# Kernel optimization log

Hardware: AMD Instinct MI355X
Metric: run time of the kernel (lower is better)

Reference implementation:

```python
import jax, jax.numpy as jnp
import numpy as np

E = 640000
N_AGENTS = 50000
D = 128
NUM_S = 50000


def setup_inputs() -> dict:
    key = jax.random.key(0)
    k1, k2, k3 = jax.random.split(key, 3)
    edge_weights = jax.random.uniform(k1, (E,), dtype=jnp.float32)
    agent_features = jax.random.normal(k2, (N_AGENTS, D), dtype=jnp.float32)
    edge_index = jax.random.randint(k3, (2, E), 0, NUM_S, dtype=jnp.int64)
    return {
        "edge_weights": edge_weights,
        "agent_features": agent_features,
        "edge_index": edge_index,
        "num_s": NUM_S,
    }


def reference(edge_weights, agent_features, edge_index, num_s):
    s_idx = edge_index[0]
    a_idx = edge_index[1]
    # gather per-edge agent features: [E, D]
    eaf = agent_features[a_idx]
    # weighted scatter-add: per-source feature sums [num_s, D] and weight sums [num_s]
    sum_wf = jax.ops.segment_sum(edge_weights[:, None] * eaf, s_idx, num_segments=num_s)
    sum_w = jax.ops.segment_sum(edge_weights, s_idx, num_segments=num_s)
    mean_per_s = sum_wf / (sum_w[:, None] + 1e-8)
    # second pass: weighted squared deviation per edge, scattered per source
    sq_diff = jnp.sum((eaf - mean_per_s[s_idx]) ** 2, axis=1)  # [E]
    var_per_s = jax.ops.segment_sum(edge_weights * sq_diff, s_idx, num_segments=num_s)
    valid = sum_w > 0
    n_valid = jnp.sum(valid)
    loss = jnp.sum(jnp.where(valid, var_per_s, 0.0)) / jnp.maximum(n_valid, 1).astype(var_per_s.dtype)
    return jnp.where(n_valid > 0, loss, jnp.asarray(0.0, var_per_s.dtype))
```

## Files before the change

### kernel.cpp

```cpp
#include <hip/hip_runtime.h>
#include <hip/hip_fp16.h>


#define D  128
#define NS 50000
#define KMAX 64
#define NBINS 391
#define BIN_CAP 2048

typedef unsigned long long ull;
typedef float f32x2 __attribute__((ext_vector_type(2)));


__global__ void prep_kernel(const float* __restrict__ af, unsigned char* __restrict__ af_q,
                            float* __restrict__ sqnorm, float* __restrict__ accum,
                            int* __restrict__ done, unsigned* __restrict__ binCursor,
                            int num_a) {
    int gtid   = blockIdx.x * 256 + threadIdx.x;
    int stride = gridDim.x * 256;
    if (gtid == 0) { accum[0] = 0.f; accum[1] = 0.f; *done = 0; }
    for (int b = gtid; b < NBINS; b += stride)
        binCursor[b * 16] = (unsigned)b * BIN_CAP;

    for (int u = gtid; u < num_a * 16; u += stride) {
        int a    = u >> 4;
        int comp = (u & 15) << 3;
        const float* src = af + (size_t)a * D + comp;
        float4 v0 = *reinterpret_cast<const float4*>(src);
        float4 v1 = *reinterpret_cast<const float4*>(src + 4);
        unsigned lo = __builtin_amdgcn_cvt_pk_fp8_f32(v0.x, v0.y, 0u, false);
        lo = __builtin_amdgcn_cvt_pk_fp8_f32(v0.z, v0.w, lo, true);
        unsigned hi = __builtin_amdgcn_cvt_pk_fp8_f32(v1.x, v1.y, 0u, false);
        hi = __builtin_amdgcn_cvt_pk_fp8_f32(v1.z, v1.w, hi, true);
        int p  = comp >> 6;
        int cc = comp & 63;
        *reinterpret_cast<ull*>(af_q + ((size_t)p * num_a + a) * 64 + cc) =
            ((ull)hi << 32) | (ull)lo;

        f32x2 q0 = __builtin_amdgcn_cvt_pk_f32_fp8(lo, false);
        f32x2 q1 = __builtin_amdgcn_cvt_pk_f32_fp8(lo, true);
        f32x2 q2 = __builtin_amdgcn_cvt_pk_f32_fp8(hi, false);
        f32x2 q3 = __builtin_amdgcn_cvt_pk_f32_fp8(hi, true);
        float ss = q0.x*q0.x + q0.y*q0.y + q1.x*q1.x + q1.y*q1.y
                 + q2.x*q2.x + q2.y*q2.y + q3.x*q3.x + q3.y*q3.y;
        #pragma unroll
        for (int m = 1; m <= 8; m <<= 1) ss += __shfl_xor(ss, m, 64);
        if ((u & 15) == 0) sqnorm[a] = ss;
    }
}


__global__ __launch_bounds__(256) void bin_pass(
    const int* __restrict__ s_idx,
    const int* __restrict__ a_idx,
    const float* __restrict__ ew,
    unsigned* __restrict__ binCursor,
    ull* __restrict__ coarse, int E)
{
    __shared__ unsigned hist[NBINS];
    __shared__ unsigned base[NBINS];
    int nb    = gridDim.x;
    int chunk = (E + nb - 1) / nb;
    int e0    = blockIdx.x * chunk;
    int e1    = min(E, e0 + chunk);

    for (int t = threadIdx.x; t < NBINS; t += 256) hist[t] = 0;
    __syncthreads();
    for (int i = e0 + (int)threadIdx.x; i < e1; i += 256)
        atomicAdd(&hist[(unsigned)s_idx[i] >> 7], 1u);
    __syncthreads();
    for (int t = threadIdx.x; t < NBINS; t += 256) {
        unsigned c = hist[t];
        base[t] = c ? atomicAdd(&binCursor[t * 16], c) : 0u;
        hist[t] = 0;
    }
    __syncthreads();
    for (int i = e0 + (int)threadIdx.x; i < e1; i += 256) {
        int s = s_idx[i];
        unsigned bin = (unsigned)s >> 7;
        unsigned r   = atomicAdd(&hist[bin], 1u);
        unsigned pos = base[bin] + r;
        if (pos < (bin + 1) * BIN_CAP) {
            unsigned low = ((unsigned)a_idx[i] << 16)
                         | (unsigned)__half_as_ushort(__float2half(ew[i]));
            coarse[pos] = ((ull)((unsigned)s & 127u) << 32) | (ull)low;
        }
    }
}


__global__ __launch_bounds__(256) void final_bucket(
    const ull* __restrict__ coarse,
    const unsigned* __restrict__ binCursor,
    unsigned* __restrict__ bucket, int* __restrict__ cnt, int num_s)
{
    __shared__ unsigned lcnt[128];
    int b = blockIdx.x;
    if (threadIdx.x < 128) lcnt[threadIdx.x] = 0;
    __syncthreads();
    unsigned start = (unsigned)b * BIN_CAP;
    unsigned end   = min(binCursor[b * 16], start + BIN_CAP);
    for (unsigned i = start + threadIdx.x; i < end; i += 256) {
        ull e = coarse[i];
        unsigned s7 = (unsigned)(e >> 32);
        unsigned r  = atomicAdd(&lcnt[s7], 1u);
        if (r < KMAX) {
            int s = b * 128 + (int)s7;
            bucket[((size_t)s << 6) + r] = (unsigned)e;
        }
    }
    __syncthreads();
    if (threadIdx.x < 128) {
        int s = b * 128 + (int)threadIdx.x;
        if (s < num_s) cnt[s] = (int)lcnt[threadIdx.x];
    }
}

__device__ __forceinline__ void fma16(const uint4& x, float w, float* acc) {
    f32x2 t;
    t = __builtin_amdgcn_cvt_pk_f32_fp8(x.x, false); acc[0]  += w*t.x; acc[1]  += w*t.y;
    t = __builtin_amdgcn_cvt_pk_f32_fp8(x.x, true);  acc[2]  += w*t.x; acc[3]  += w*t.y;
    t = __builtin_amdgcn_cvt_pk_f32_fp8(x.y, false); acc[4]  += w*t.x; acc[5]  += w*t.y;
    t = __builtin_amdgcn_cvt_pk_f32_fp8(x.y, true);  acc[6]  += w*t.x; acc[7]  += w*t.y;
    t = __builtin_amdgcn_cvt_pk_f32_fp8(x.z, false); acc[8]  += w*t.x; acc[9]  += w*t.y;
    t = __builtin_amdgcn_cvt_pk_f32_fp8(x.z, true);  acc[10] += w*t.x; acc[11] += w*t.y;
    t = __builtin_amdgcn_cvt_pk_f32_fp8(x.w, false); acc[12] += w*t.x; acc[13] += w*t.y;
    t = __builtin_amdgcn_cvt_pk_f32_fp8(x.w, true);  acc[14] += w*t.x; acc[15] += w*t.y;
}


__global__ __launch_bounds__(256) void slice_merged(
    const unsigned char* __restrict__ af_q,
    const float* __restrict__ sqnorm,
    const unsigned* __restrict__ bucket,
    const int* __restrict__ cnt,
    float* __restrict__ fn2a, float* __restrict__ fn2b,
    float* __restrict__ s2acc, float* __restrict__ wsumv,
    int num_s, int num_a)
{
    const bool p0  = (blockIdx.x & 1u) == 0u;
    const unsigned char* afp = af_q + (p0 ? 0 : (size_t)num_a * 64);
    int lblk    = blockIdx.x >> 1;
    int gid     = lblk * 256 + threadIdx.x;
    int group   = gid >> 5;
    int lane    = threadIdx.x & 31;
    int j       = lane >> 2;
    int ccq     = lane & 3;
    int ngroups = ((gridDim.x >> 1) * 256) >> 5;

    for (int s0 = group * 2; s0 < num_s; s0 += ngroups * 2) {
        int s1 = s0 + 1;
        int2 c2 = *reinterpret_cast<const int2*>(cnt + s0);
        int c0 = min(c2.x, KMAX);
        int c1 = min(c2.y, KMAX);
        const unsigned* b0 = bucket + ((size_t)s0 << 6);
        const unsigned* b1 = bucket + ((size_t)s1 << 6);

        float accA[16] = {};
        float accB[16] = {};
        float s2A = 0.f, wlA = 0.f, s2B = 0.f, wlB = 0.f;

        int cmax  = max(c0, c1);
        int iters = (cmax + 15) >> 4;
        for (int it = 0; it < iters; ++it) {
            int idxA = it * 16 + j;
            int idxB = idxA + 8;
            unsigned wa0  = (idxA < c0) ? b0[idxA] : 0u;
            unsigned wa0b = (idxB < c0) ? b0[idxB] : 0u;
            unsigned wa1  = (idxA < c1) ? b1[idxA] : 0u;
            unsigned wa1b = (idxB < c1) ? b1[idxB] : 0u;
            float w0  = __half2float(__ushort_as_half((unsigned short)(wa0  & 0xFFFFu)));
            float w0b = __half2float(__ushort_as_half((unsigned short)(wa0b & 0xFFFFu)));
            float w1  = __half2float(__ushort_as_half((unsigned short)(wa1  & 0xFFFFu)));
            float w1b = __half2float(__ushort_as_half((unsigned short)(wa1b & 0xFFFFu)));
            int A0  = (int)(wa0  >> 16);
            int A0b = (int)(wa0b >> 16);
            int A1  = (int)(wa1  >> 16);
            int A1b = (int)(wa1b >> 16);
            uint4 x  = *reinterpret_cast<const uint4*>(afp + ((size_t)A0  << 6) + (ccq << 4));
            uint4 xb = *reinterpret_cast<const uint4*>(afp + ((size_t)A0b << 6) + (ccq << 4));
            uint4 y  = *reinterpret_cast<const uint4*>(afp + ((size_t)A1  << 6) + (ccq << 4));
            uint4 yb = *reinterpret_cast<const uint4*>(afp + ((size_t)A1b << 6) + (ccq << 4));
            fma16(x,  w0,  accA);
            fma16(xb, w0b, accA);
            fma16(y,  w1,  accB);
            fma16(yb, w1b, accB);
            if (p0 && ccq == 0) {
                s2A += w0 * sqnorm[A0] + w0b * sqnorm[A0b];  wlA += w0 + w0b;
                s2B += w1 * sqnorm[A1] + w1b * sqnorm[A1b];  wlB += w1 + w1b;
            }
        }
        #pragma unroll
        for (int m = 4; m <= 16; m <<= 1) {
            #pragma unroll
            for (int k = 0; k < 16; ++k) {
                accA[k] += __shfl_xor(accA[k], m, 64);
                accB[k] += __shfl_xor(accB[k], m, 64);
            }
            if (p0) {
                s2A += __shfl_xor(s2A, m, 64); wlA += __shfl_xor(wlA, m, 64);
                s2B += __shfl_xor(s2B, m, 64); wlB += __shfl_xor(wlB, m, 64);
            }
        }
        float n2a = 0.f, n2b = 0.f;
        #pragma unroll
        for (int k = 0; k < 16; ++k) { n2a += accA[k] * accA[k]; n2b += accB[k] * accB[k]; }
        n2a += __shfl_xor(n2a, 1, 64); n2a += __shfl_xor(n2a, 2, 64);
        n2b += __shfl_xor(n2b, 1, 64); n2b += __shfl_xor(n2b, 2, 64);
        if (lane == 0) {
            if (p0) {
                fn2a[s0] = n2a;  s2acc[s0] = s2A;  wsumv[s0] = wlA;
                fn2a[s1] = n2b;  s2acc[s1] = s2B;  wsumv[s1] = wlB;
            } else {
                fn2b[s0] = n2a;
                fn2b[s1] = n2b;
            }
        }
    }
}


__global__ void loss_finalize(const float* __restrict__ fn2a, const float* __restrict__ fn2b,
                              const float* __restrict__ s2acc, const float* __restrict__ wsumv,
                              float* __restrict__ accum, int* __restrict__ done,
                              float* __restrict__ out, int num_s) {
    __shared__ float sv[4], sc[4];
    float lv = 0.f, lc = 0.f;
    for (int s = blockIdx.x * blockDim.x + threadIdx.x; s < num_s; s += gridDim.x * blockDim.x) {
        float w = wsumv[s];
        if (w > 0.f) {
            float n2  = fn2a[s] + fn2b[s];
            float inv = 1.f / (w + 1e-8f);
            lv += s2acc[s] - n2 * inv * (2.f - w * inv);
            lc += 1.f;
        }
    }
    #pragma unroll
    for (int m = 1; m < 64; m <<= 1) { lv += __shfl_xor(lv, m, 64); lc += __shfl_xor(lc, m, 64); }
    int wv = threadIdx.x >> 6;
    if ((threadIdx.x & 63) == 0) { sv[wv] = lv; sc[wv] = lc; }
    __syncthreads();
    if (threadIdx.x == 0) {
        atomicAdd(accum + 0, sv[0] + sv[1] + sv[2] + sv[3]);
        atomicAdd(accum + 1, sc[0] + sc[1] + sc[2] + sc[3]);
        __threadfence();
        unsigned t = atomicAdd((unsigned*)done, 1u);
        if (t == gridDim.x - 1) {
            float v = atomicAdd(accum + 0, 0.f);
            float c = atomicAdd(accum + 1, 0.f);
            out[0] = (c > 0.f) ? (v / fmaxf(c, 1.f)) : 0.f;
        }
    }
}

extern "C" void kernel_launch(void* const* d_in, const int* in_sizes, int n_in,
                              void* d_out, int out_size, void* d_ws, size_t ws_size,
                              hipStream_t stream) {
    const float* ew = (const float*)d_in[0];
    const float* af = (const float*)d_in[1];
    const int*   ei = (const int*)d_in[2];
    const int E     = in_sizes[0];
    const int num_a = in_sizes[1] / D;
    const int num_s = NS;

    const int* s_idx = ei;
    const int* a_idx = ei + E;

    char* ws = (char*)d_ws;
    size_t off = 0;
    auto alloc = [&](size_t bytes, size_t align) -> char* {
        off = (off + align - 1) & ~(align - 1);
        char* p = ws + off;
        off += bytes;
        return p;
    };
    int*   cnt    = (int*)alloc((size_t)(num_s + 4) * 4, 16);
    float* accum  = (float*)(cnt + num_s);
    int*   done   = (int*)(cnt + num_s + 2);
    float* fn2a   = (float*)alloc((size_t)num_s * 4, 16);
    float* fn2b   = (float*)alloc((size_t)num_s * 4, 16);
    float* s2acc  = (float*)alloc((size_t)num_s * 4, 16);
    float* wsumv  = (float*)alloc((size_t)num_s * 4, 16);
    float* sqnorm = (float*)alloc((size_t)num_a * 4, 16);
    unsigned* binCursor = (unsigned*)alloc((size_t)NBINS * 16 * 4, 64);
    unsigned char* af_q = (unsigned char*)alloc((size_t)2 * num_a * 64, 256);
    unsigned* bucket = (unsigned*)alloc((size_t)num_s * KMAX * 4, 512);
    ull* coarse = (ull*)alloc((size_t)NBINS * BIN_CAP * 8, 512);

    prep_kernel<<<(num_a * 16 + 255) / 256, 256, 0, stream>>>(af, af_q, sqnorm, accum, done,
                                                              binCursor, num_a);
    bin_pass<<<256, 256, 0, stream>>>(s_idx, a_idx, ew, binCursor, coarse, E);
    final_bucket<<<NBINS, 256, 0, stream>>>(coarse, binCursor, bucket, cnt, num_s);
    slice_merged<<<4096, 256, 0, stream>>>(af_q, sqnorm, bucket, cnt,
                                           fn2a, fn2b, s2acc, wsumv, num_s, num_a);
    loss_finalize<<<128, 256, 0, stream>>>(fn2a, fn2b, s2acc, wsumv, accum, done,
                                           (float*)d_out, num_s);
}
```

Baseline: 79.51 us.

## Fuse final bucketing into slice kernel via shared-memory counting sort per bin

Removes the separate final_bucket kernel and the global bucket/cnt arrays. Each bin_slice block reloads its coarse bin, counting-sorts entries by source in LDS with a wave prefix scan, and then accumulates features straight from shared memory. This drops a launch and a global write/read round trip, and also lifts the per-source KMAX cap. In exchange, both half-blocks of a bin redo the sort, and the grid shrinks from 4096 to 782 blocks, which may reduce latency hiding for the gathers.

```diff
diff --git a/kernel.cpp b/kernel.cpp
--- a/kernel.cpp
+++ b/kernel.cpp
@@ -4,7 +4,6 @@
 
 #define D  128
 #define NS 50000
-#define KMAX 64
 #define NBINS 391
 #define BIN_CAP 2048
 
@@ -88,34 +87,6 @@
     }
 }
 
-
-__global__ __launch_bounds__(256) void final_bucket(
-    const ull* __restrict__ coarse,
-    const unsigned* __restrict__ binCursor,
-    unsigned* __restrict__ bucket, int* __restrict__ cnt, int num_s)
-{
-    __shared__ unsigned lcnt[128];
-    int b = blockIdx.x;
-    if (threadIdx.x < 128) lcnt[threadIdx.x] = 0;
-    __syncthreads();
-    unsigned start = (unsigned)b * BIN_CAP;
-    unsigned end   = min(binCursor[b * 16], start + BIN_CAP);
-    for (unsigned i = start + threadIdx.x; i < end; i += 256) {
-        ull e = coarse[i];
-        unsigned s7 = (unsigned)(e >> 32);
-        unsigned r  = atomicAdd(&lcnt[s7], 1u);
-        if (r < KMAX) {
-            int s = b * 128 + (int)s7;
-            bucket[((size_t)s << 6) + r] = (unsigned)e;
-        }
-    }
-    __syncthreads();
-    if (threadIdx.x < 128) {
-        int s = b * 128 + (int)threadIdx.x;
-        if (s < num_s) cnt[s] = (int)lcnt[threadIdx.x];
-    }
-}
-
 __device__ __forceinline__ void fma16(const uint4& x, float w, float* acc) {
     f32x2 t;
     t = __builtin_amdgcn_cvt_pk_f32_fp8(x.x, false); acc[0]  += w*t.x; acc[1]  += w*t.y;
@@ -129,32 +100,65 @@
 }
 
 
-__global__ __launch_bounds__(256) void slice_merged(
+__global__ __launch_bounds__(256) void bin_slice(
+    const ull* __restrict__ coarse,
+    const unsigned* __restrict__ binCursor,
     const unsigned char* __restrict__ af_q,
     const float* __restrict__ sqnorm,
-    const unsigned* __restrict__ bucket,
-    const int* __restrict__ cnt,
     float* __restrict__ fn2a, float* __restrict__ fn2b,
     float* __restrict__ s2acc, float* __restrict__ wsumv,
     int num_s, int num_a)
 {
+    __shared__ unsigned sorted[BIN_CAP];
+    __shared__ unsigned lcnt[128];
+    __shared__ unsigned loff[128];
+    __shared__ unsigned lcur[128];
+
     const bool p0  = (blockIdx.x & 1u) == 0u;
+    const int  bin = blockIdx.x >> 1;
     const unsigned char* afp = af_q + (p0 ? 0 : (size_t)num_a * 64);
-    int lblk    = blockIdx.x >> 1;
-    int gid     = lblk * 256 + threadIdx.x;
-    int group   = gid >> 5;
-    int lane    = threadIdx.x & 31;
-    int j       = lane >> 2;
-    int ccq     = lane & 3;
-    int ngroups = ((gridDim.x >> 1) * 256) >> 5;
-
-    for (int s0 = group * 2; s0 < num_s; s0 += ngroups * 2) {
-        int s1 = s0 + 1;
-        int2 c2 = *reinterpret_cast<const int2*>(cnt + s0);
-        int c0 = min(c2.x, KMAX);
-        int c1 = min(c2.y, KMAX);
-        const unsigned* b0 = bucket + ((size_t)s0 << 6);
-        const unsigned* b1 = bucket + ((size_t)s1 << 6);
+    const int tid = threadIdx.x;
+
+    const unsigned start = (unsigned)bin * BIN_CAP;
+    const unsigned n = min(binCursor[bin * 16] - start, (unsigned)BIN_CAP);
+
+    if (tid < 128) lcnt[tid] = 0;
+    __syncthreads();
+    for (unsigned i = tid; i < n; i += 256)
+        atomicAdd(&lcnt[(unsigned)(coarse[start + i] >> 32)], 1u);
+    __syncthreads();
+    if (tid < 64) {
+        unsigned v0 = lcnt[tid], v1 = lcnt[64 + tid];
+        unsigned i0 = v0, i1 = v1;
+        #pragma unroll
+        for (int d = 1; d < 64; d <<= 1) {
+            unsigned t0 = __shfl_up(i0, d, 64);
+            unsigned t1 = __shfl_up(i1, d, 64);
+            if (tid >= d) { i0 += t0; i1 += t1; }
+        }
+        unsigned tot0 = __shfl(i0, 63, 64);
+        loff[tid]      = i0 - v0;         lcur[tid]      = i0 - v0;
+        loff[64 + tid] = tot0 + i1 - v1;  lcur[64 + tid] = tot0 + i1 - v1;
+    }
+    __syncthreads();
+    for (unsigned i = tid; i < n; i += 256) {
+        ull e = coarse[start + i];
+        unsigned r = atomicAdd(&lcur[(unsigned)(e >> 32)], 1u);
+        sorted[r] = (unsigned)e;
+    }
+    __syncthreads();
+
+    int group = tid >> 5;
+    int lane  = tid & 31;
+    int j     = lane >> 2;
+    int ccq   = lane & 3;
+
+    for (int p = 0; p < 8; ++p) {
+        int s7a = group * 16 + p * 2;
+        int sA  = bin * 128 + s7a;
+        if (sA >= num_s) break;
+        int c0 = (int)lcnt[s7a], c1 = (int)lcnt[s7a + 1];
+        int base0 = (int)loff[s7a], base1 = (int)loff[s7a + 1];
 
         float accA[16] = {};
         float accB[16] = {};
@@ -165,10 +169,10 @@
         for (int it = 0; it < iters; ++it) {
             int idxA = it * 16 + j;
             int idxB = idxA + 8;
-            unsigned wa0  = (idxA < c0) ? b0[idxA] : 0u;
-            unsigned wa0b = (idxB < c0) ? b0[idxB] : 0u;
-            unsigned wa1  = (idxA < c1) ? b1[idxA] : 0u;
-            unsigned wa1b = (idxB < c1) ? b1[idxB] : 0u;
+            unsigned wa0  = (idxA < c0) ? sorted[base0 + idxA] : 0u;
+            unsigned wa0b = (idxB < c0) ? sorted[base0 + idxB] : 0u;
+            unsigned wa1  = (idxA < c1) ? sorted[base1 + idxA] : 0u;
+            unsigned wa1b = (idxB < c1) ? sorted[base1 + idxB] : 0u;
             float w0  = __half2float(__ushort_as_half((unsigned short)(wa0  & 0xFFFFu)));
             float w0b = __half2float(__ushort_as_half((unsigned short)(wa0b & 0xFFFFu)));
             float w1  = __half2float(__ushort_as_half((unsigned short)(wa1  & 0xFFFFu)));
@@ -209,11 +213,11 @@
         n2b += __shfl_xor(n2b, 1, 64); n2b += __shfl_xor(n2b, 2, 64);
         if (lane == 0) {
             if (p0) {
-                fn2a[s0] = n2a;  s2acc[s0] = s2A;  wsumv[s0] = wlA;
-                fn2a[s1] = n2b;  s2acc[s1] = s2B;  wsumv[s1] = wlB;
+                fn2a[sA]     = n2a;  s2acc[sA]     = s2A;  wsumv[sA]     = wlA;
+                fn2a[sA + 1] = n2b;  s2acc[sA + 1] = s2B;  wsumv[sA + 1] = wlB;
             } else {
-                fn2b[s0] = n2a;
-                fn2b[s1] = n2b;
+                fn2b[sA]     = n2a;
+                fn2b[sA + 1] = n2b;
             }
         }
     }
@@ -274,9 +278,8 @@
         off += bytes;
         return p;
     };
-    int*   cnt    = (int*)alloc((size_t)(num_s + 4) * 4, 16);
-    float* accum  = (float*)(cnt + num_s);
-    int*   done   = (int*)(cnt + num_s + 2);
+    float* accum  = (float*)alloc(4 * 4, 16);
+    int*   done   = (int*)(accum + 2);
     float* fn2a   = (float*)alloc((size_t)num_s * 4, 16);
     float* fn2b   = (float*)alloc((size_t)num_s * 4, 16);
     float* s2acc  = (float*)alloc((size_t)num_s * 4, 16);
@@ -284,15 +287,13 @@
     float* sqnorm = (float*)alloc((size_t)num_a * 4, 16);
     unsigned* binCursor = (unsigned*)alloc((size_t)NBINS * 16 * 4, 64);
     unsigned char* af_q = (unsigned char*)alloc((size_t)2 * num_a * 64, 256);
-    unsigned* bucket = (unsigned*)alloc((size_t)num_s * KMAX * 4, 512);
     ull* coarse = (ull*)alloc((size_t)NBINS * BIN_CAP * 8, 512);
 
     prep_kernel<<<(num_a * 16 + 255) / 256, 256, 0, stream>>>(af, af_q, sqnorm, accum, done,
                                                               binCursor, num_a);
     bin_pass<<<256, 256, 0, stream>>>(s_idx, a_idx, ew, binCursor, coarse, E);
-    final_bucket<<<NBINS, 256, 0, stream>>>(coarse, binCursor, bucket, cnt, num_s);
-    slice_merged<<<4096, 256, 0, stream>>>(af_q, sqnorm, bucket, cnt,
-                                           fn2a, fn2b, s2acc, wsumv, num_s, num_a);
+    bin_slice<<<NBINS * 2, 256, 0, stream>>>(coarse, binCursor, af_q, sqnorm,
+                                             fn2a, fn2b, s2acc, wsumv, num_s, num_a);
     loss_finalize<<<128, 256, 0, stream>>>(fn2a, fn2b, s2acc, wsumv, accum, done,
                                            (float*)d_out, num_s);
 }
```

Result: slower. 88.47 us (+11.3%).

## Fuse prep and binning kernels, replace global bin cursors with per-block slots

Applied to the files above, without the earlier changes.

Merges the fp8 quantization prep kernel and the coarse binning pass into one launch: the first 256 blocks bin edges while the remaining blocks quantize agent features. Global atomic bin cursors are replaced by fixed per-(bin, block) slots of capacity 32 with a count table, which removes the cursor init and the global atomics. final_bucket now has each thread walk one block's slot serially. This saves a launch and the contention on shared cursors, but uses a larger coarse buffer, loses edges silently past 32 per slot, and gives final_bucket uneven per-thread serial loops.

```diff
diff --git a/kernel.cpp b/kernel.cpp
--- a/kernel.cpp
+++ b/kernel.cpp
@@ -6,84 +6,81 @@
 #define NS 50000
 #define KMAX 64
 #define NBINS 391
-#define BIN_CAP 2048
+#define CAP_PB 32
 
 typedef unsigned long long ull;
 typedef float f32x2 __attribute__((ext_vector_type(2)));
 
 
-__global__ void prep_kernel(const float* __restrict__ af, unsigned char* __restrict__ af_q,
-                            float* __restrict__ sqnorm, float* __restrict__ accum,
-                            int* __restrict__ done, unsigned* __restrict__ binCursor,
-                            int num_a) {
-    int gtid   = blockIdx.x * 256 + threadIdx.x;
-    int stride = gridDim.x * 256;
-    if (gtid == 0) { accum[0] = 0.f; accum[1] = 0.f; *done = 0; }
-    for (int b = gtid; b < NBINS; b += stride)
-        binCursor[b * 16] = (unsigned)b * BIN_CAP;
-
-    for (int u = gtid; u < num_a * 16; u += stride) {
-        int a    = u >> 4;
-        int comp = (u & 15) << 3;
-        const float* src = af + (size_t)a * D + comp;
-        float4 v0 = *reinterpret_cast<const float4*>(src);
-        float4 v1 = *reinterpret_cast<const float4*>(src + 4);
-        unsigned lo = __builtin_amdgcn_cvt_pk_fp8_f32(v0.x, v0.y, 0u, false);
-        lo = __builtin_amdgcn_cvt_pk_fp8_f32(v0.z, v0.w, lo, true);
-        unsigned hi = __builtin_amdgcn_cvt_pk_fp8_f32(v1.x, v1.y, 0u, false);
-        hi = __builtin_amdgcn_cvt_pk_fp8_f32(v1.z, v1.w, hi, true);
-        int p  = comp >> 6;
-        int cc = comp & 63;
-        *reinterpret_cast<ull*>(af_q + ((size_t)p * num_a + a) * 64 + cc) =
-            ((ull)hi << 32) | (ull)lo;
-
-        f32x2 q0 = __builtin_amdgcn_cvt_pk_f32_fp8(lo, false);
-        f32x2 q1 = __builtin_amdgcn_cvt_pk_f32_fp8(lo, true);
-        f32x2 q2 = __builtin_amdgcn_cvt_pk_f32_fp8(hi, false);
-        f32x2 q3 = __builtin_amdgcn_cvt_pk_f32_fp8(hi, true);
-        float ss = q0.x*q0.x + q0.y*q0.y + q1.x*q1.x + q1.y*q1.y
-                 + q2.x*q2.x + q2.y*q2.y + q3.x*q3.x + q3.y*q3.y;
-        #pragma unroll
-        for (int m = 1; m <= 8; m <<= 1) ss += __shfl_xor(ss, m, 64);
-        if ((u & 15) == 0) sqnorm[a] = ss;
-    }
-}
-
-
-__global__ __launch_bounds__(256) void bin_pass(
-    const int* __restrict__ s_idx,
-    const int* __restrict__ a_idx,
+__global__ __launch_bounds__(256) void prep_bin(
+    const float* __restrict__ af, unsigned char* __restrict__ af_q,
+    float* __restrict__ sqnorm, float* __restrict__ accum, int* __restrict__ done,
+    const int* __restrict__ s_idx, const int* __restrict__ a_idx,
     const float* __restrict__ ew,
-    unsigned* __restrict__ binCursor,
-    ull* __restrict__ coarse, int E)
+    unsigned* __restrict__ blkCnt,
+    ull* __restrict__ coarse,
+    int E, int num_a)
 {
     __shared__ unsigned hist[NBINS];
-    __shared__ unsigned base[NBINS];
-    int nb    = gridDim.x;
-    int chunk = (E + nb - 1) / nb;
-    int e0    = blockIdx.x * chunk;
-    int e1    = min(E, e0 + chunk);
-
-    for (int t = threadIdx.x; t < NBINS; t += 256) hist[t] = 0;
-    __syncthreads();
-    for (int i = e0 + (int)threadIdx.x; i < e1; i += 256)
-        atomicAdd(&hist[(unsigned)s_idx[i] >> 7], 1u);
-    __syncthreads();
-    for (int t = threadIdx.x; t < NBINS; t += 256) {
-        unsigned c = hist[t];
-        base[t] = c ? atomicAdd(&binCursor[t * 16], c) : 0u;
-        hist[t] = 0;
-    }
-    __syncthreads();
-    for (int i = e0 + (int)threadIdx.x; i < e1; i += 256) {
-        int s = s_idx[i];
-        unsigned bin = (unsigned)s >> 7;
-        unsigned r   = atomicAdd(&hist[bin], 1u);
-        unsigned pos = base[bin] + r;
-        if (pos < (bin + 1) * BIN_CAP) {
-            unsigned low = ((unsigned)a_idx[i] << 16)
-                         | (unsigned)__half_as_ushort(__float2half(ew[i]));
-            coarse[pos] = ((ull)((unsigned)s & 127u) << 32) | (ull)low;
+    const int tid = threadIdx.x;
+
+    if (blockIdx.x < 256) {
+        const int b     = blockIdx.x;
+        const int chunk = (E + 255) / 256;
+        const int e0    = b * chunk;
+        const int e1    = min(E, e0 + chunk);
+
+        for (int t = tid; t < NBINS; t += 256) hist[t] = 0;
+        __syncthreads();
+        for (int i = e0 + tid; i < e1; i += 256)
+            atomicAdd(&hist[(unsigned)s_idx[i] >> 7], 1u);
+        __syncthreads();
+        for (int t = tid; t < NBINS; t += 256) {
+            blkCnt[t * 256 + b] = min(hist[t], (unsigned)CAP_PB);
+            hist[t] = 0;
+        }
+        __syncthreads();
+        for (int i = e0 + tid; i < e1; i += 256) {
+            int s = s_idx[i];
+            unsigned bin = (unsigned)s >> 7;
+            unsigned r   = atomicAdd(&hist[bin], 1u);
+            if (r < CAP_PB) {
+                unsigned low = ((unsigned)a_idx[i] << 16)
+                             | (unsigned)__half_as_ushort(__float2half(ew[i]));
+                coarse[((size_t)bin * 256 + b) * CAP_PB + r] =
+                    ((ull)((unsigned)s & 127u) << 32) | (ull)low;
+            }
+        }
+    } else {
+        int pb     = blockIdx.x - 256;
+        int gtid   = pb * 256 + tid;
+        int stride = ((int)gridDim.x - 256) * 256;
+        if (gtid == 0) { accum[0] = 0.f; accum[1] = 0.f; *done = 0; }
+
+        for (int u = gtid; u < num_a * 16; u += stride) {
+            int a    = u >> 4;
+            int comp = (u & 15) << 3;
+            const float* src = af + (size_t)a * D + comp;
+            float4 v0 = *reinterpret_cast<const float4*>(src);
+            float4 v1 = *reinterpret_cast<const float4*>(src + 4);
+            unsigned lo = __builtin_amdgcn_cvt_pk_fp8_f32(v0.x, v0.y, 0u, false);
+            lo = __builtin_amdgcn_cvt_pk_fp8_f32(v0.z, v0.w, lo, true);
+            unsigned hi = __builtin_amdgcn_cvt_pk_fp8_f32(v1.x, v1.y, 0u, false);
+            hi = __builtin_amdgcn_cvt_pk_fp8_f32(v1.z, v1.w, hi, true);
+            int p  = comp >> 6;
+            int cc = comp & 63;
+            *reinterpret_cast<ull*>(af_q + ((size_t)p * num_a + a) * 64 + cc) =
+                ((ull)hi << 32) | (ull)lo;
+
+            f32x2 q0 = __builtin_amdgcn_cvt_pk_f32_fp8(lo, false);
+            f32x2 q1 = __builtin_amdgcn_cvt_pk_f32_fp8(lo, true);
+            f32x2 q2 = __builtin_amdgcn_cvt_pk_f32_fp8(hi, false);
+            f32x2 q3 = __builtin_amdgcn_cvt_pk_f32_fp8(hi, true);
+            float ss = q0.x*q0.x + q0.y*q0.y + q1.x*q1.x + q1.y*q1.y
+                     + q2.x*q2.x + q2.y*q2.y + q3.x*q3.x + q3.y*q3.y;
+            #pragma unroll
+            for (int m = 1; m <= 8; m <<= 1) ss += __shfl_xor(ss, m, 64);
+            if ((u & 15) == 0) sqnorm[a] = ss;
         }
     }
 }
@@ -91,28 +88,29 @@
 
 __global__ __launch_bounds__(256) void final_bucket(
     const ull* __restrict__ coarse,
-    const unsigned* __restrict__ binCursor,
+    const unsigned* __restrict__ blkCnt,
     unsigned* __restrict__ bucket, int* __restrict__ cnt, int num_s)
 {
     __shared__ unsigned lcnt[128];
-    int b = blockIdx.x;
-    if (threadIdx.x < 128) lcnt[threadIdx.x] = 0;
+    int bin = blockIdx.x;
+    int tid = threadIdx.x;
+    if (tid < 128) lcnt[tid] = 0;
     __syncthreads();
-    unsigned start = (unsigned)b * BIN_CAP;
-    unsigned end   = min(binCursor[b * 16], start + BIN_CAP);
-    for (unsigned i = start + threadIdx.x; i < end; i += 256) {
-        ull e = coarse[i];
+    unsigned c = blkCnt[bin * 256 + tid];
+    const ull* reg = coarse + ((size_t)bin * 256 + tid) * CAP_PB;
+    for (unsigned r = 0; r < c; ++r) {
+        ull e = reg[r];
         unsigned s7 = (unsigned)(e >> 32);
-        unsigned r  = atomicAdd(&lcnt[s7], 1u);
-        if (r < KMAX) {
-            int s = b * 128 + (int)s7;
-            bucket[((size_t)s << 6) + r] = (unsigned)e;
+        unsigned k  = atomicAdd(&lcnt[s7], 1u);
+        if (k < KMAX) {
+            int s = bin * 128 + (int)s7;
+            bucket[((size_t)s << 6) + k] = (unsigned)e;
         }
     }
     __syncthreads();
-    if (threadIdx.x < 128) {
-        int s = b * 128 + (int)threadIdx.x;
-        if (s < num_s) cnt[s] = (int)lcnt[threadIdx.x];
+    if (tid < 128) {
+        int s = bin * 128 + tid;
+        if (s < num_s) cnt[s] = (int)min(lcnt[tid], (unsigned)KMAX);
     }
 }
 
@@ -274,23 +272,24 @@
         off += bytes;
         return p;
     };
-    int*   cnt    = (int*)alloc((size_t)(num_s + 4) * 4, 16);
-    float* accum  = (float*)(cnt + num_s);
-    int*   done   = (int*)(cnt + num_s + 2);
+    float* accum  = (float*)alloc(4 * 4, 16);
+    int*   done   = (int*)(accum + 2);
+    int*   cnt    = (int*)alloc((size_t)num_s * 4, 16);
     float* fn2a   = (float*)alloc((size_t)num_s * 4, 16);
     float* fn2b   = (float*)alloc((size_t)num_s * 4, 16);
     float* s2acc  = (float*)alloc((size_t)num_s * 4, 16);
     float* wsumv  = (float*)alloc((size_t)num_s * 4, 16);
     float* sqnorm = (float*)alloc((size_t)num_a * 4, 16);
-    unsigned* binCursor = (unsigned*)alloc((size_t)NBINS * 16 * 4, 64);
+    unsigned* blkCnt    = (unsigned*)alloc((size_t)NBINS * 256 * 4, 64);
     unsigned char* af_q = (unsigned char*)alloc((size_t)2 * num_a * 64, 256);
-    unsigned* bucket = (unsigned*)alloc((size_t)num_s * KMAX * 4, 512);
-    ull* coarse = (ull*)alloc((size_t)NBINS * BIN_CAP * 8, 512);
-
-    prep_kernel<<<(num_a * 16 + 255) / 256, 256, 0, stream>>>(af, af_q, sqnorm, accum, done,
-                                                              binCursor, num_a);
-    bin_pass<<<256, 256, 0, stream>>>(s_idx, a_idx, ew, binCursor, coarse, E);
-    final_bucket<<<NBINS, 256, 0, stream>>>(coarse, binCursor, bucket, cnt, num_s);
+    unsigned* bucket    = (unsigned*)alloc((size_t)num_s * KMAX * 4, 512);
+    ull* coarse = (ull*)alloc((size_t)NBINS * 256 * CAP_PB * 8, 512);
+
+    int prep_blocks = (num_a * 16 + 255) / 256;
+    prep_bin<<<256 + prep_blocks, 256, 0, stream>>>(af, af_q, sqnorm, accum, done,
+                                                    s_idx, a_idx, ew, blkCnt, coarse,
+                                                    E, num_a);
+    final_bucket<<<NBINS, 256, 0, stream>>>(coarse, blkCnt, bucket, cnt, num_s);
     slice_merged<<<4096, 256, 0, stream>>>(af_q, sqnorm, bucket, cnt,
                                            fn2a, fn2b, s2acc, wsumv, num_s, num_a);
     loss_finalize<<<128, 256, 0, stream>>>(fn2a, fn2b, s2acc, wsumv, accum, done,
```

Measured after the change: 71.56 us. 1.11x faster.
